# Kernel optimization log

Measured on AMD Instinct MI355X. Metric: run time of the kernel, lower is better.

## Reference

```python
import jax, jax.numpy as jnp
import numpy as np

N_NODES = 100000
N_EDGES = 1600000
D_IN, D_HID, D_OUT = 512, 256, 32


def setup_inputs() -> dict:
    key = jax.random.key(0)
    ks = jax.random.split(key, 8)
    features = jax.random.normal(ks[0], (N_NODES, D_IN), dtype=jnp.float32)
    A_data = jax.random.uniform(ks[1], (N_EDGES,), dtype=jnp.float32)
    A_row = jax.random.randint(ks[2], (N_EDGES,), 0, N_NODES, dtype=jnp.int32)
    A_col = jax.random.randint(ks[3], (N_EDGES,), 0, N_NODES, dtype=jnp.int32)
    # MLP params (glorot-ish scaling)
    W1 = jax.random.normal(ks[4], (D_IN, D_HID), dtype=jnp.float32) * (1.0 / np.sqrt(D_IN))
    b1 = jnp.zeros((D_HID,), dtype=jnp.float32)
    W2 = jax.random.normal(ks[5], (D_HID, D_OUT), dtype=jnp.float32) * (1.0 / np.sqrt(D_HID))
    b2 = jnp.zeros((D_OUT,), dtype=jnp.float32)
    return {"features": features, "A_data": A_data, "W1": W1, "b1": b1,
            "W2": W2, "b2": b2, "A_row": A_row, "A_col": A_col}


def reference(features, A_data, W1, b1, W2, b2, A_row, A_col):
    # head_transform: 2-layer MLP (is_training=False -> dropout identity)
    h = jax.nn.relu(features @ W1 + b1)          # [N, D_HID]
    X = h @ W2 + b2                              # [N, D_OUT]
    # propagator dropout: rate=0.0 / eval mode -> identity on A
    # sparse COO A @ X: gather columns, scale by edge values, scatter-add to rows
    msgs = A_data[:, None] * X[A_col]            # [E, D_OUT]
    out = jax.ops.segment_sum(msgs, A_row, num_segments=N_NODES)  # [N, D_OUT]
    return out
```

## Files before the change

### kernel.cpp

```cpp
#include <hip/hip_runtime.h>
#include <hip/hip_bf16.h>

typedef __bf16 bf16;
typedef __attribute__((ext_vector_type(8))) __bf16 bf16x8;
typedef __attribute__((ext_vector_type(4))) float f32x4;

constexpr int D_IN  = 512;
constexpr int D_HID = 256;
constexpr int D_OUT = 32;
constexpr int BM = 64;
constexpr int BK = 32;
constexpr int HPAD = 260;
constexpr int SCAN_VPT  = 8;
constexpr int SCAN_SPAN = 2048;
constexpr int NSLICE = 8;

#define GLOBAL_AS(p) ((const __attribute__((address_space(1))) void*)(p))
#define LDS_AS(p)    ((__attribute__((address_space(3))) void*)(p))

__global__ __launch_bounds__(256) void prep_kernel(
    const float* __restrict__ W1, const float* __restrict__ W2,
    bf16* __restrict__ W1T, bf16* __restrict__ W2T)
{
    int idx = blockIdx.x * 256 + threadIdx.x;
    if (idx < D_IN * D_HID) {
        int k = idx / D_HID, n = idx % D_HID;
        W1T[n * D_IN + k] = (bf16)W1[idx];
    }
    int j = idx - D_IN * D_HID;
    if (j >= 0 && j < D_HID * D_OUT) {
        int k = j / D_OUT, n = j % D_OUT;
        W2T[n * D_HID + k] = (bf16)W2[j];
    }
}

__global__ __launch_bounds__(256) void fused_mlp_kernel(
    const float* __restrict__ feat,
    const bf16* __restrict__ W1T, const bf16* __restrict__ W2T,
    const float* __restrict__ b1, const float* __restrict__ b2,
    float* __restrict__ X, int N)
{
    __shared__ __align__(16) char smem[BM * HPAD * sizeof(bf16)];
    bf16* Bsm  = (bf16*)smem;
    bf16* Hsm  = (bf16*)smem;

    const int tid  = threadIdx.x;
    const int wave = tid >> 6;
    const int lane = tid & 63;
    const int ln   = lane & 15;
    const int q    = lane >> 4;
    const int mw   = wave * 16;
    const int r0   = blockIdx.x * BM;

    f32x4 acc[16] = {};

    const long arow = (long)min(r0 + mw + ln, N - 1);
    const float* asrc = feat + arow * D_IN + q * 8;

    const int psl = q ^ ((ln >> 1) & 3);

    for (int k0 = 0; k0 < D_IN; k0 += BK) {
        #pragma unroll
        for (int i = 0; i < 4; ++i) {
            int c  = i * 256 + wave * 64 + lane;
            int sl = (c & 3) ^ ((c >> 3) & 3);
            const bf16* gsrc = W1T + ((c >> 2) * D_IN + k0 + sl * 8);
            bf16* lbase = Bsm + (i * 256 + wave * 64) * 8;
            __builtin_amdgcn_global_load_lds(GLOBAL_AS(gsrc), LDS_AS(lbase), 16, 0, 0);
        }

        float4 f0 = *(const float4*)(asrc + k0);
        float4 f1 = *(const float4*)(asrc + k0 + 4);
        bf16x8 af;
        af[0] = (bf16)f0.x; af[1] = (bf16)f0.y; af[2] = (bf16)f0.z; af[3] = (bf16)f0.w;
        af[4] = (bf16)f1.x; af[5] = (bf16)f1.y; af[6] = (bf16)f1.z; af[7] = (bf16)f1.w;

        __syncthreads();

        #pragma unroll
        for (int t = 0; t < 16; ++t) {
            bf16x8 bfv = *(const bf16x8*)&Bsm[(t * 16 + ln) * BK + psl * 8];
            acc[t] = __builtin_amdgcn_mfma_f32_16x16x32_bf16(af, bfv, acc[t], 0, 0, 0);
        }
        __syncthreads();
    }

    #pragma unroll
    for (int t = 0; t < 16; ++t) {
        int colh = t * 16 + ln;
        float bb = b1[colh];
        #pragma unroll
        for (int i = 0; i < 4; ++i) {
            int row = mw + q * 4 + i;
            float v = acc[t][i] + bb;
            Hsm[row * HPAD + colh] = (bf16)fmaxf(v, 0.0f);
        }
    }
    __syncthreads();

    f32x4 acc2[2] = {};
    #pragma unroll
    for (int k0 = 0; k0 < D_HID; k0 += BK) {
        bf16x8 af2 = *(const bf16x8*)&Hsm[(mw + ln) * HPAD + k0 + q * 8];
        #pragma unroll
        for (int t = 0; t < 2; ++t) {
            bf16x8 bfv = *(const bf16x8*)&W2T[(t * 16 + ln) * D_HID + k0 + q * 8];
            acc2[t] = __builtin_amdgcn_mfma_f32_16x16x32_bf16(af2, bfv, acc2[t], 0, 0, 0);
        }
    }

    #pragma unroll
    for (int t = 0; t < 2; ++t) {
        int c = t * 16 + ln;
        float bb = b2[c];
        #pragma unroll
        for (int i = 0; i < 4; ++i) {
            int row = r0 + mw + q * 4 + i;
            if (row < N) X[row * D_OUT + c] = acc2[t][i] + bb;
        }
    }
}

__global__ __launch_bounds__(256) void hist_kernel(
    const int* __restrict__ Arow, int* __restrict__ counts, int E)
{
    int e = blockIdx.x * 256 + threadIdx.x;
    if (e < E) atomicAdd(&counts[Arow[e]], 1);
}

__global__ __launch_bounds__(256) void scanA_kernel(
    const int* __restrict__ counts, int* __restrict__ offs,
    int* __restrict__ partials, int N)
{
    __shared__ int lds[256];
    int t = threadIdx.x;
    int base = blockIdx.x * SCAN_SPAN + t * SCAN_VPT;
    int v[SCAN_VPT];
    int tsum = 0;
    #pragma unroll
    for (int j = 0; j < SCAN_VPT; ++j) {
        v[j] = (base + j < N) ? counts[base + j] : 0;
        tsum += v[j];
    }
    lds[t] = tsum;
    __syncthreads();
    for (int d = 1; d < 256; d <<= 1) {
        int x = (t >= d) ? lds[t - d] : 0;
        __syncthreads();
        lds[t] += x;
        __syncthreads();
    }
    int run = lds[t] - tsum;
    #pragma unroll
    for (int j = 0; j < SCAN_VPT; ++j) {
        if (base + j < N) offs[base + j] = run;
        run += v[j];
    }
    if (t == 255) partials[blockIdx.x] = lds[255];
}

__global__ __launch_bounds__(256) void scanB_kernel(int* __restrict__ partials, int nb)
{
    __shared__ int lds[256];
    int t = threadIdx.x;
    int v = (t < nb) ? partials[t] : 0;
    lds[t] = v;
    __syncthreads();
    for (int d = 1; d < 256; d <<= 1) {
        int x = (t >= d) ? lds[t - d] : 0;
        __syncthreads();
        lds[t] += x;
        __syncthreads();
    }
    if (t < nb) partials[t] = lds[t] - v;
}

__global__ __launch_bounds__(256) void scanC_kernel(
    int* __restrict__ offs, const int* __restrict__ partials,
    int* __restrict__ cursor, int N)
{
    int i = blockIdx.x * 256 + threadIdx.x;
    if (i < N) {
        int o = offs[i] + partials[i / SCAN_SPAN];
        offs[i] = o;
        cursor[i] = o;
    }
}

__global__ __launch_bounds__(256) void reorder_kernel(
    const int* __restrict__ Arow, const int* __restrict__ Acol,
    const float* __restrict__ Adata, int* __restrict__ cursor,
    int2* __restrict__ pairs, int E, int rps)
{
    int b = blockIdx.x;
    int slice = b & (NSLICE - 1);
    int e = (b >> 3) * 256 + threadIdx.x;
    if (e >= E) return;
    int r = Arow[e];
    if ((unsigned)(r - slice * rps) >= (unsigned)rps) return;
    int p = atomicAdd(&cursor[r], 1);
    int2 pk;
    pk.x = Acol[e];
    pk.y = __float_as_int(Adata[e]);
    pairs[p] = pk;
}

__global__ __launch_bounds__(256) void reduce_kernel(
    const int* __restrict__ offs, const int* __restrict__ counts,
    const int2* __restrict__ pairs, const float* __restrict__ X,
    float* __restrict__ out, int N)
{
    int w    = threadIdx.x >> 6;
    int lane = threadIdx.x & 63;
    int r    = blockIdx.x * 4 + w;
    if (r >= N) return;
    int slot = lane >> 3;
    int dg   = lane & 7;
    int off  = offs[r];
    int deg  = counts[r];
    f32x4 acc = {0.0f, 0.0f, 0.0f, 0.0f};
    for (int i = slot; i < deg; i += 8) {
        int2  pk = pairs[off + i];
        float a  = __int_as_float(pk.y);
        f32x4 x  = *(const f32x4*)(X + (long)pk.x * D_OUT + dg * 4);
        acc += a * x;
    }
    #pragma unroll
    for (int d = 8; d < 64; d <<= 1) {
        acc[0] += __shfl_xor(acc[0], d, 64);
        acc[1] += __shfl_xor(acc[1], d, 64);
        acc[2] += __shfl_xor(acc[2], d, 64);
        acc[3] += __shfl_xor(acc[3], d, 64);
    }
    if (slot == 0) *(f32x4*)(out + (long)r * D_OUT + dg * 4) = acc;
}

__global__ __launch_bounds__(256) void scatter_kernel(
    const float* __restrict__ Adata, const int* __restrict__ Arow,
    const int* __restrict__ Acol, const float* __restrict__ X,
    float* __restrict__ out, int E)
{
    int idx = blockIdx.x * 256 + threadIdx.x;
    int e = idx >> 3;
    int g = idx & 7;
    if (e >= E) return;
    int   col = Acol[e];
    int   row = Arow[e];
    float a   = Adata[e];
    float4 x = *(const float4*)(X + (long)col * D_OUT + g * 4);
    float* o = out + (long)row * D_OUT + g * 4;
    unsafeAtomicAdd(o + 0, a * x.x);
    unsafeAtomicAdd(o + 1, a * x.y);
    unsafeAtomicAdd(o + 2, a * x.z);
    unsafeAtomicAdd(o + 3, a * x.w);
}

extern "C" void kernel_launch(void* const* d_in, const int* in_sizes, int n_in,
                              void* d_out, int out_size, void* d_ws, size_t ws_size,
                              hipStream_t stream)
{
    const float* feat  = (const float*)d_in[0];
    const float* Adata = (const float*)d_in[1];
    const float* W1    = (const float*)d_in[2];
    const float* b1    = (const float*)d_in[3];
    const float* W2    = (const float*)d_in[4];
    const float* b2    = (const float*)d_in[5];
    const int*   Arow  = (const int*)d_in[6];
    const int*   Acol  = (const int*)d_in[7];

    const int N = in_sizes[0] / D_IN;
    const int E = in_sizes[1];

    char* p = (char*)d_ws;
    auto alloc = [&](size_t bytes) {
        char* q = p;
        p += (bytes + 255) & ~(size_t)255;
        return q;
    };
    float* X       = (float*)alloc((size_t)N * D_OUT * sizeof(float));
    bf16*  W1T     = (bf16*) alloc((size_t)D_IN * D_HID * sizeof(bf16));
    bf16*  W2T     = (bf16*) alloc((size_t)D_HID * D_OUT * sizeof(bf16));
    int*   counts  = (int*)  alloc((size_t)N * sizeof(int));
    int*   offs    = (int*)  alloc((size_t)N * sizeof(int));
    int*   cursor  = (int*)  alloc((size_t)N * sizeof(int));
    int*   partials= (int*)  alloc(256 * sizeof(int));
    int2*  pairs   = (int2*) alloc((size_t)E * sizeof(int2));
    size_t need = (size_t)(p - (char*)d_ws);
    const bool use_csr = (need <= ws_size);

    float* out = (float*)d_out;

    int prep_elems = D_IN * D_HID + D_HID * D_OUT;
    prep_kernel<<<(prep_elems + 255) / 256, 256, 0, stream>>>(W1, W2, W1T, W2T);

    fused_mlp_kernel<<<(N + BM - 1) / BM, 256, 0, stream>>>(
        feat, W1T, W2T, b1, b2, X, N);

    if (use_csr) {
        hipMemsetAsync(counts, 0, (size_t)N * sizeof(int), stream);
        hist_kernel<<<(E + 255) / 256, 256, 0, stream>>>(Arow, counts, E);
        int nb = (N + SCAN_SPAN - 1) / SCAN_SPAN;
        scanA_kernel<<<nb, 256, 0, stream>>>(counts, offs, partials, N);
        scanB_kernel<<<1, 256, 0, stream>>>(partials, nb);
        scanC_kernel<<<(N + 255) / 256, 256, 0, stream>>>(offs, partials, cursor, N);
        int rps = (N + NSLICE - 1) / NSLICE;
        reorder_kernel<<<NSLICE * ((E + 255) / 256), 256, 0, stream>>>(
            Arow, Acol, Adata, cursor, pairs, E, rps);
        reduce_kernel<<<(N + 3) / 4, 256, 0, stream>>>(
            offs, counts, pairs, X, out, N);
    } else {
        hipMemsetAsync(out, 0, (size_t)out_size * sizeof(float), stream);
        long scatter_threads = (long)E * 8;
        scatter_kernel<<<(scatter_threads + 255) / 256, 256, 0, stream>>>(
            Adata, Arow, Acol, X, out, E);
    }
}
```

Baseline: 535.5 us.

## Double MLP K-tile, chunk hidden staging in LDS, slice histogram atomics by row

The first GEMM now loads 64-wide K tiles of W1 with an 8-way XOR swizzle, which halves the number of barrier pairs per K loop. The hidden activations are no longer staged as one full 64x256 tile. They are written 32 columns at a time into a small padded buffer and fed straight into the second GEMM. This cuts LDS to 32KB, which could raise occupancy, at the cost of extra barriers in the epilogue. The histogram kernel is also split into 8 row slices, each block pass filtering edges by row range, to localize atomics. That costs 8x more reads of A_row.

```diff
diff --git a/kernel.cpp b/kernel.cpp
--- a/kernel.cpp
+++ b/kernel.cpp
@@ -9,8 +9,8 @@
 constexpr int D_HID = 256;
 constexpr int D_OUT = 32;
 constexpr int BM = 64;
-constexpr int BK = 32;
-constexpr int HPAD = 260;
+constexpr int BK = 64;
+constexpr int HCP = 40;
 constexpr int SCAN_VPT  = 8;
 constexpr int SCAN_SPAN = 2048;
 constexpr int NSLICE = 8;
@@ -40,9 +40,9 @@
     const float* __restrict__ b1, const float* __restrict__ b2,
     float* __restrict__ X, int N)
 {
-    __shared__ __align__(16) char smem[BM * HPAD * sizeof(bf16)];
-    bf16* Bsm  = (bf16*)smem;
-    bf16* Hsm  = (bf16*)smem;
+    __shared__ __align__(16) char smem[D_HID * BK * sizeof(bf16)];
+    bf16* Bsm = (bf16*)smem;
+    bf16* Hc  = (bf16*)smem;
 
     const int tid  = threadIdx.x;
     const int wave = tid >> 6;
@@ -57,56 +57,70 @@
     const long arow = (long)min(r0 + mw + ln, N - 1);
     const float* asrc = feat + arow * D_IN + q * 8;
 
-    const int psl = q ^ ((ln >> 1) & 3);
-
     for (int k0 = 0; k0 < D_IN; k0 += BK) {
         #pragma unroll
-        for (int i = 0; i < 4; ++i) {
+        for (int i = 0; i < 8; ++i) {
             int c  = i * 256 + wave * 64 + lane;
-            int sl = (c & 3) ^ ((c >> 3) & 3);
-            const bf16* gsrc = W1T + ((c >> 2) * D_IN + k0 + sl * 8);
+            int sl = (c & 7) ^ ((c >> 3) & 7);
+            const bf16* gsrc = W1T + ((c >> 3) * D_IN + k0 + sl * 8);
             bf16* lbase = Bsm + (i * 256 + wave * 64) * 8;
             __builtin_amdgcn_global_load_lds(GLOBAL_AS(gsrc), LDS_AS(lbase), 16, 0, 0);
         }
 
-        float4 f0 = *(const float4*)(asrc + k0);
-        float4 f1 = *(const float4*)(asrc + k0 + 4);
-        bf16x8 af;
-        af[0] = (bf16)f0.x; af[1] = (bf16)f0.y; af[2] = (bf16)f0.z; af[3] = (bf16)f0.w;
-        af[4] = (bf16)f1.x; af[5] = (bf16)f1.y; af[6] = (bf16)f1.z; af[7] = (bf16)f1.w;
-
-        __syncthreads();
-
+        bf16x8 af0, af1;
+        {
+            float4 f0 = *(const float4*)(asrc + k0);
+            float4 f1 = *(const float4*)(asrc + k0 + 4);
+            af0[0] = (bf16)f0.x; af0[1] = (bf16)f0.y; af0[2] = (bf16)f0.z; af0[3] = (bf16)f0.w;
+            af0[4] = (bf16)f1.x; af0[5] = (bf16)f1.y; af0[6] = (bf16)f1.z; af0[7] = (bf16)f1.w;
+            float4 f2 = *(const float4*)(asrc + k0 + 32);
+            float4 f3 = *(const float4*)(asrc + k0 + 36);
+            af1[0] = (bf16)f2.x; af1[1] = (bf16)f2.y; af1[2] = (bf16)f2.z; af1[3] = (bf16)f2.w;
+            af1[4] = (bf16)f3.x; af1[5] = (bf16)f3.y; af1[6] = (bf16)f3.z; af1[7] = (bf16)f3.w;
+        }
+
+        __syncthreads();
+
+        {
+            const int psl0 = (0 * 4 + q) ^ (ln & 7);
+            #pragma unroll
+            for (int t = 0; t < 16; ++t) {
+                bf16x8 bfv = *(const bf16x8*)&Bsm[(t * 16 + ln) * BK + psl0 * 8];
+                acc[t] = __builtin_amdgcn_mfma_f32_16x16x32_bf16(af0, bfv, acc[t], 0, 0, 0);
+            }
+            const int psl1 = (1 * 4 + q) ^ (ln & 7);
+            #pragma unroll
+            for (int t = 0; t < 16; ++t) {
+                bf16x8 bfv = *(const bf16x8*)&Bsm[(t * 16 + ln) * BK + psl1 * 8];
+                acc[t] = __builtin_amdgcn_mfma_f32_16x16x32_bf16(af1, bfv, acc[t], 0, 0, 0);
+            }
+        }
+        __syncthreads();
+    }
+
+    f32x4 acc2[2] = {};
+    #pragma unroll
+    for (int cc = 0; cc < 8; ++cc) {
         #pragma unroll
-        for (int t = 0; t < 16; ++t) {
-            bf16x8 bfv = *(const bf16x8*)&Bsm[(t * 16 + ln) * BK + psl * 8];
-            acc[t] = __builtin_amdgcn_mfma_f32_16x16x32_bf16(af, bfv, acc[t], 0, 0, 0);
-        }
-        __syncthreads();
-    }
-
-    #pragma unroll
-    for (int t = 0; t < 16; ++t) {
-        int colh = t * 16 + ln;
-        float bb = b1[colh];
+        for (int tt = 0; tt < 2; ++tt) {
+            int t = cc * 2 + tt;
+            float bb = b1[t * 16 + ln];
+            #pragma unroll
+            for (int i = 0; i < 4; ++i) {
+                int row = mw + q * 4 + i;
+                float v = acc[t][i] + bb;
+                Hc[row * HCP + tt * 16 + ln] = (bf16)fmaxf(v, 0.0f);
+            }
+        }
+        __syncthreads();
+        bf16x8 af2 = *(const bf16x8*)&Hc[(mw + ln) * HCP + q * 8];
+        int kg = cc * 32 + q * 8;
         #pragma unroll
-        for (int i = 0; i < 4; ++i) {
-            int row = mw + q * 4 + i;
-            float v = acc[t][i] + bb;
-            Hsm[row * HPAD + colh] = (bf16)fmaxf(v, 0.0f);
-        }
-    }
-    __syncthreads();
-
-    f32x4 acc2[2] = {};
-    #pragma unroll
-    for (int k0 = 0; k0 < D_HID; k0 += BK) {
-        bf16x8 af2 = *(const bf16x8*)&Hsm[(mw + ln) * HPAD + k0 + q * 8];
-        #pragma unroll
-        for (int t = 0; t < 2; ++t) {
-            bf16x8 bfv = *(const bf16x8*)&W2T[(t * 16 + ln) * D_HID + k0 + q * 8];
-            acc2[t] = __builtin_amdgcn_mfma_f32_16x16x32_bf16(af2, bfv, acc2[t], 0, 0, 0);
-        }
+        for (int t2 = 0; t2 < 2; ++t2) {
+            bf16x8 bfv = *(const bf16x8*)&W2T[(t2 * 16 + ln) * D_HID + kg];
+            acc2[t2] = __builtin_amdgcn_mfma_f32_16x16x32_bf16(af2, bfv, acc2[t2], 0, 0, 0);
+        }
+        __syncthreads();
     }
 
     #pragma unroll
@@ -122,10 +136,15 @@
 }
 
 __global__ __launch_bounds__(256) void hist_kernel(
-    const int* __restrict__ Arow, int* __restrict__ counts, int E)
-{
-    int e = blockIdx.x * 256 + threadIdx.x;
-    if (e < E) atomicAdd(&counts[Arow[e]], 1);
+    const int* __restrict__ Arow, int* __restrict__ counts, int E, int rps)
+{
+    int b = blockIdx.x;
+    int slice = b & (NSLICE - 1);
+    int e = (b >> 3) * 256 + threadIdx.x;
+    if (e >= E) return;
+    int r = Arow[e];
+    if ((unsigned)(r - slice * rps) >= (unsigned)rps) return;
+    atomicAdd(&counts[r], 1);
 }
 
 __global__ __launch_bounds__(256) void scanA_kernel(
@@ -298,12 +317,13 @@
 
     if (use_csr) {
         hipMemsetAsync(counts, 0, (size_t)N * sizeof(int), stream);
-        hist_kernel<<<(E + 255) / 256, 256, 0, stream>>>(Arow, counts, E);
+        int rps = (N + NSLICE - 1) / NSLICE;
+        hist_kernel<<<NSLICE * ((E + 255) / 256), 256, 0, stream>>>(
+            Arow, counts, E, rps);
         int nb = (N + SCAN_SPAN - 1) / SCAN_SPAN;
         scanA_kernel<<<nb, 256, 0, stream>>>(counts, offs, partials, N);
         scanB_kernel<<<1, 256, 0, stream>>>(partials, nb);
         scanC_kernel<<<(N + 255) / 256, 256, 0, stream>>>(offs, partials, cursor, N);
-        int rps = (N + NSLICE - 1) / NSLICE;
         reorder_kernel<<<NSLICE * ((E + 255) / 256), 256, 0, stream>>>(
             Arow, Acol, Adata, cursor, pairs, E, rps);
         reduce_kernel<<<(N + 3) / 4, 256, 0, stream>>>(
```

New measurement: 532.5 us. No clear change (-0.6%).
